# Kernel tuning notes

Hardware: AMD Instinct MI355X
Metric: run time of the kernel (lower is better)

## Reference

```python
import jax, jax.numpy as jnp
import numpy as np

N_NODES = 100000
N_EDGES = 1600000
N_GRAPHS = 4096
GN_EPS = 1e-5
SLOPE = 0.01  # torch leaky_relu default negative_slope


def _graph_norm(x, w, b, s):
    # PyG GraphNorm with batch=None: single-graph normalization over all nodes
    mean = jnp.mean(x, axis=0, keepdims=True)
    out = x - s * mean
    var = jnp.mean(out * out, axis=0, keepdims=True)
    return w * out * jax.lax.rsqrt(var + GN_EPS) + b


def setup_inputs() -> dict:
    key = jax.random.key(0)
    ks = jax.random.split(key, 12)

    def rn(k, shape, fan_in):
        return (jax.random.normal(k, shape, jnp.float32) / np.float32(np.sqrt(fan_in)))

    return {
        "x": jax.random.normal(ks[0], (N_NODES, 48), jnp.float32),
        "edge_attr": jax.random.normal(ks[1], (N_EDGES, 10), jnp.float32),
        # GINConv MLP layer 0: Linear(48->128); layers 1..3: Linear(128->128)
        "W1_0": rn(ks[2], (48, 128), 48), "b1_0": jnp.zeros((128,), jnp.float32),
        "W1_rest": rn(ks[3], (3, 128, 128), 128), "b1_rest": jnp.zeros((3, 128), jnp.float32),
        # GraphNorm inside each MLP (weight, bias, mean_scale)
        "gn_w": jnp.ones((4, 128), jnp.float32), "gn_b": jnp.zeros((4, 128), jnp.float32), "gn_s": jnp.ones((4, 128), jnp.float32),
        # second Linear of each MLP (128->128; last conv maps to out_channels=128)
        "W2": rn(ks[4], (4, 128, 128), 128), "b2": jnp.zeros((4, 128), jnp.float32),
        # BasicGNN post-conv GraphNorms (after layers 0..2 only)
        "pn_w": jnp.ones((3, 128), jnp.float32), "pn_b": jnp.zeros((3, 128), jnp.float32), "pn_s": jnp.ones((3, 128), jnp.float32),
        # readout MLP head
        "fc1_W": rn(ks[5], (384, 64), 384), "fc1_b": jnp.zeros((64,), jnp.float32),
        "fc2_W": rn(ks[6], (64, 3), 64), "fc2_b": jnp.zeros((3,), jnp.float32),
        "edge_index": jax.random.randint(ks[7], (2, N_EDGES), 0, N_NODES),
        "batch": jnp.sort(jax.random.randint(ks[8], (N_NODES,), 0, N_GRAPHS)),
    }


def reference(x, edge_attr, W1_0, b1_0, W1_rest, b1_rest, gn_w, gn_b, gn_s,
              W2, b2, pn_w, pn_b, pn_s, fc1_W, fc1_b, fc2_W, fc2_b,
              edge_index, batch):
    # edge_attr is ignored: PyG GIN does not support edge attributes.
    src, dst = edge_index[0], edge_index[1]
    h = x
    for i in range(4):
        # GINConv: mlp((1+eps)*x_i + sum_{j in N(i)} x_j), eps = 0
        agg = jax.ops.segment_sum(h[src], dst, num_segments=N_NODES)
        m = h + agg
        if i == 0:
            m = m @ W1_0 + b1_0
        else:
            m = m @ W1_rest[i - 1] + b1_rest[i - 1]
        m = _graph_norm(m, gn_w[i], gn_b[i], gn_s[i])  # norm inside MLP
        m = jax.nn.leaky_relu(m, SLOPE)
        h = m @ W2[i] + b2[i]
        if i < 3:  # BasicGNN: norm + act after every conv except the last
            h = _graph_norm(h, pn_w[i], pn_b[i], pn_s[i])
            h = jax.nn.leaky_relu(h, SLOPE)

    # global mean / add / max pooling over data.batch
    sums = jax.ops.segment_sum(h, batch, num_segments=N_GRAPHS)
    cnt = jax.ops.segment_sum(jnp.ones((h.shape[0], 1), h.dtype), batch,
                              num_segments=N_GRAPHS)
    mean = sums / jnp.maximum(cnt, 1.0)
    mx = jax.ops.segment_max(h, batch, num_segments=N_GRAPHS)
    mx = jnp.where(jnp.isfinite(mx), mx, 0.0)  # guard empty segments

    g = jnp.concatenate([mean, sums, mx], axis=1)  # [G, 384]
    g = jax.nn.leaky_relu(g @ fc1_W + fc1_b, SLOPE)
    return g @ fc2_W + fc2_b  # [G, 3]
```

## Files before the change

### kernel.cpp

```cpp
#include <hip/hip_runtime.h>
#include <hip/hip_bf16.h>
#include <math.h>

#define N_NODES  100000
#define N_EDGES  1600000
#define N_GRAPHS 4096
#define NBUCKET  ((N_NODES + 127) / 128)
#define NPART    256
#define ROWBLKS_AL 6256

typedef __attribute__((ext_vector_type(4))) float f32x4;
typedef __attribute__((ext_vector_type(8))) short bf16x8;

__device__ __forceinline__ float lrelu(float x) { return fmaxf(x, 0.01f * x); }

__device__ __forceinline__ unsigned short f2bf(float f) {
    unsigned u = __float_as_uint(f);
    unsigned r = (u + 0x7FFFu + ((u >> 16) & 1u)) >> 16;
    return (unsigned short)r;
}
__device__ __forceinline__ float bf2f(unsigned short h) {
    return __uint_as_float(((unsigned)h) << 16);
}

__global__ __launch_bounds__(1024) void scan_kernel(const unsigned* __restrict__ in,
                                                    unsigned* __restrict__ out, int n) {
    __shared__ unsigned wsum[16];
    __shared__ unsigned carry_s;
    int t = threadIdx.x, lane = t & 63, wv = t >> 6;
    if (t == 0) carry_s = 0u;
    __syncthreads();
    for (int base = 0; base < n; base += 4096) {
        unsigned carry = carry_s;
        unsigned v[4]; unsigned s = 0u;
#pragma unroll
        for (int i = 0; i < 4; ++i) {
            int idx = base + t * 4 + i;
            v[i] = (idx < n) ? in[idx] : 0u;
            s += v[i];
        }
        unsigned ps = s;
#pragma unroll
        for (int off = 1; off < 64; off <<= 1) {
            unsigned x = __shfl_up(ps, off, 64);
            if (lane >= off) ps += x;
        }
        if (lane == 63) wsum[wv] = ps;
        __syncthreads();
        if (wv == 0 && lane < 16) {
            unsigned pw = wsum[lane];
#pragma unroll
            for (int off = 1; off < 16; off <<= 1) {
                unsigned x = __shfl_up(pw, off, 64);
                if (lane >= off) pw += x;
            }
            wsum[lane] = pw;
        }
        __syncthreads();
        unsigned wbase = wv ? wsum[wv - 1] : 0u;
        unsigned run = carry + wbase + (ps - s);
#pragma unroll
        for (int i = 0; i < 4; ++i) {
            int idx = base + t * 4 + i;
            if (idx < n) out[idx] = run;
            run += v[i];
        }
        unsigned total = wsum[15];
        __syncthreads();
        if (t == 0) carry_s = carry + total;
        __syncthreads();
    }
    if (t == 0) out[n] = carry_s;
}

__global__ __launch_bounds__(256) void phist_kernel(const int* __restrict__ dst,
        unsigned* __restrict__ cnt, int E, int chunk) {
    __shared__ unsigned lc[NBUCKET];
    int p = blockIdx.x, t = threadIdx.x;
    for (int i = t; i < NBUCKET; i += 256) lc[i] = 0u;
    __syncthreads();
    int e0 = p * chunk, e1 = e0 + chunk; if (e1 > E) e1 = E;
    for (int e = e0 + t; e < e1; e += 256)
        atomicAdd(&lc[((unsigned)dst[e]) >> 7], 1u);
    __syncthreads();
    for (int i = t; i < NBUCKET; i += 256) cnt[(size_t)p * NBUCKET + i] = lc[i];
}

__global__ void btot_kernel(const unsigned* __restrict__ cnt, unsigned* __restrict__ tot) {
    int b = blockIdx.x * 256 + threadIdx.x;
    if (b >= NBUCKET) return;
    unsigned s = 0u;
    for (int p = 0; p < NPART; ++p) s += cnt[(size_t)p * NBUCKET + b];
    tot[b] = s;
}

__global__ __launch_bounds__(256) void poff_kernel(unsigned* __restrict__ cnt,
        const unsigned* __restrict__ bucket_base) {
    int b = blockIdx.x * 4 + (threadIdx.x >> 6);
    if (b >= NBUCKET) return;
    int lane = threadIdx.x & 63;
    unsigned v[4]; unsigned s = 0u;
#pragma unroll
    for (int i = 0; i < 4; ++i) {
        int p = lane * 4 + i;
        v[i] = cnt[(size_t)p * NBUCKET + b];
        s += v[i];
    }
    unsigned ps = s;
#pragma unroll
    for (int off = 1; off < 64; off <<= 1) {
        unsigned x = __shfl_up(ps, off, 64);
        if (lane >= off) ps += x;
    }
    unsigned run = bucket_base[b] + (ps - s);
#pragma unroll
    for (int i = 0; i < 4; ++i) {
        int p = lane * 4 + i;
        cnt[(size_t)p * NBUCKET + b] = run;
        run += v[i];
    }
}

__global__ __launch_bounds__(256) void pscat_kernel(const int* __restrict__ ei,
        const unsigned* __restrict__ cnt, unsigned* __restrict__ pair, int E, int chunk) {
    __shared__ unsigned lcur[NBUCKET];
    int p = blockIdx.x, t = threadIdx.x;
    for (int i = t; i < NBUCKET; i += 256) lcur[i] = cnt[(size_t)p * NBUCKET + i];
    __syncthreads();
    int e0 = p * chunk, e1 = e0 + chunk; if (e1 > E) e1 = E;
    for (int e = e0 + t; e < e1; e += 256) {
        unsigned src = (unsigned)ei[e];
        unsigned dst = (unsigned)ei[E + e];
        unsigned b = dst >> 7;
        unsigned pos = atomicAdd(&lcur[b], 1u);
        pair[pos] = src | ((dst & 127u) << 20);
    }
}

__global__ __launch_bounds__(256) void fillc2_kernel(const unsigned* __restrict__ pair,
        const unsigned* __restrict__ bucket_base, unsigned* __restrict__ row_ptr,
        unsigned* __restrict__ col, int N) {
    __shared__ unsigned lcnt[128], lpre[128], lcur[128];
    int b = blockIdx.x;
    int node0 = b << 7;
    int t = threadIdx.x;
    if (t < 128) { lcnt[t] = 0u; lcur[t] = 0u; }
    __syncthreads();
    unsigned bb = bucket_base[b], be = bucket_base[b + 1];
    for (unsigned i = bb + t; i < be; i += 256)
        atomicAdd(&lcnt[(pair[i] >> 20) & 127u], 1u);
    __syncthreads();
    if (t < 64) {
        unsigned v0 = lcnt[2 * t], v1 = lcnt[2 * t + 1];
        unsigned s = v0 + v1;
        unsigned ps = s;
#pragma unroll
        for (int off = 1; off < 64; off <<= 1) {
            unsigned x = __shfl_up(ps, off, 64);
            if (t >= off) ps += x;
        }
        unsigned base = ps - s;
        lpre[2 * t] = base;
        lpre[2 * t + 1] = base + v0;
    }
    __syncthreads();
    if (t < 128) {
        int node = node0 + t;
        if (node < N) row_ptr[node] = bb + lpre[t];
    }
    if (b == (int)gridDim.x - 1 && t == 0) row_ptr[N] = be;
    for (unsigned i = bb + t; i < be; i += 256) {
        unsigned u = pair[i];
        unsigned d = (u >> 20) & 127u;
        unsigned pos = bb + lpre[d] + atomicAdd(&lcur[d], 1u);
        col[pos] = u & 0xFFFFFu;
    }
}

__global__ void gsearch_kernel(const int* __restrict__ batch, unsigned* __restrict__ gptr,
                               int N, int G) {
    int g = blockIdx.x * 256 + threadIdx.x;
    if (g > G) return;
    int lo = 0, hi = N;
    while (lo < hi) { int mid = (lo + hi) >> 1; if (batch[mid] < g) lo = mid + 1; else hi = mid; }
    gptr[g] = (unsigned)lo;
}

__global__ void cast_kernel(const float* __restrict__ in, unsigned short* __restrict__ outb, int n4) {
    int i = blockIdx.x * 256 + threadIdx.x;
    if (i >= n4) return;
    f32x4 v = *(const f32x4*)(in + (size_t)i * 4);
    uint2 u;
    u.x = (unsigned)f2bf(v[0]) | ((unsigned)f2bf(v[1]) << 16);
    u.y = (unsigned)f2bf(v[2]) | ((unsigned)f2bf(v[3]) << 16);
    *(uint2*)(outb + (size_t)i * 4) = u;
}

__global__ __launch_bounds__(256) void tfm_kernel(const unsigned short* __restrict__ hb,
        const float* __restrict__ stats, const float* __restrict__ wp,
        const float* __restrict__ bp, const float* __restrict__ sp, float invN,
        unsigned short* __restrict__ yb, int total8) {
    __shared__ float la[128], ldd[128];
    int t = threadIdx.x;
    if (t < 128) {
        float mean = stats[t] * invN;
        float ex2  = stats[128 + t] * invN;
        float sv   = sp[t];
        float var  = ex2 - 2.f * sv * mean * mean + sv * sv * mean * mean;
        float a    = wp[t] * rsqrtf(var + 1e-5f);
        la[t] = a; ldd[t] = bp[t] - a * sv * mean;
    }
    __syncthreads();
    int i = blockIdx.x * 256 + t;
    if (i >= total8) return;
    int c0 = (i & 15) * 8;
    uint4 u = *(const uint4*)(hb + (size_t)i * 8);
    unsigned uu[4] = {u.x, u.y, u.z, u.w};
    unsigned ow[4];
#pragma unroll
    for (int q = 0; q < 4; ++q) {
        int c = c0 + 2 * q;
        float v0 = lrelu(fmaf(la[c],     __uint_as_float(uu[q] << 16),         ldd[c]));
        float v1 = lrelu(fmaf(la[c + 1], __uint_as_float(uu[q] & 0xffff0000u), ldd[c + 1]));
        ow[q] = (unsigned)f2bf(v0) | ((unsigned)f2bf(v1) << 16);
    }
    uint4 o; o.x = ow[0]; o.y = ow[1]; o.z = ow[2]; o.w = ow[3];
    *(uint4*)(yb + (size_t)i * 8) = o;
}

template<int D, int KOCT>
__global__ __launch_bounds__(256) void agg_kernel(const unsigned short* __restrict__ hb, int ld_in,
        const unsigned* __restrict__ row_ptr, const unsigned* __restrict__ col,
        unsigned short* __restrict__ op, int n) {
    int node = blockIdx.x * 4 + (threadIdx.x >> 6);
    int l = threadIdx.x & 63;
    if (node >= n || l >= KOCT * 4) return;
    int c = 2 * l;
    float x0 = 0.f, x1 = 0.f;
    if (c < D) {
        const unsigned short* hp = hb + c;
#define LOADU(s) *(const unsigned*)(hp + (size_t)(s) * ld_in)
#define LO(u) __uint_as_float((u) << 16)
#define HI(u) __uint_as_float((u) & 0xffff0000u)
        unsigned su = LOADU(node);
        x0 = LO(su); x1 = HI(su);
        float y0 = 0.f, y1 = 0.f, z0 = 0.f, z1 = 0.f, q0 = 0.f, q1 = 0.f;
        unsigned e0 = row_ptr[node], e1 = row_ptr[node + 1];
        unsigned e = e0;
        for (; e + 8 <= e1; e += 8) {
            unsigned c0i = col[e],     c1i = col[e + 1], c2i = col[e + 2], c3i = col[e + 3];
            unsigned c4i = col[e + 4], c5i = col[e + 5], c6i = col[e + 6], c7i = col[e + 7];
            unsigned u0 = LOADU(c0i), u1 = LOADU(c1i), u2 = LOADU(c2i), u3 = LOADU(c3i);
            unsigned u4 = LOADU(c4i), u5 = LOADU(c5i), u6 = LOADU(c6i), u7 = LOADU(c7i);
            x0 += LO(u0); x1 += HI(u0); y0 += LO(u1); y1 += HI(u1);
            z0 += LO(u2); z1 += HI(u2); q0 += LO(u3); q1 += HI(u3);
            x0 += LO(u4); x1 += HI(u4); y0 += LO(u5); y1 += HI(u5);
            z0 += LO(u6); z1 += HI(u6); q0 += LO(u7); q1 += HI(u7);
        }
        for (; e + 4 <= e1; e += 4) {
            unsigned c0i = col[e], c1i = col[e + 1], c2i = col[e + 2], c3i = col[e + 3];
            unsigned u0 = LOADU(c0i), u1 = LOADU(c1i), u2 = LOADU(c2i), u3 = LOADU(c3i);
            x0 += LO(u0); x1 += HI(u0); y0 += LO(u1); y1 += HI(u1);
            z0 += LO(u2); z1 += HI(u2); q0 += LO(u3); q1 += HI(u3);
        }
        for (; e < e1; ++e) {
            unsigned u = LOADU(col[e]);
            x0 += LO(u); x1 += HI(u);
        }
#undef LOADU
#undef LO
#undef HI
        x0 = (x0 + y0) + (z0 + q0);
        x1 = (x1 + y1) + (z1 + q1);
    }
    unsigned outw = (unsigned)f2bf(x0) | ((unsigned)f2bf(x1) << 16);
    size_t fo = (((size_t)(node >> 4) * KOCT + (l >> 2)) * 16 + (node & 15)) * 8 + 2 * (l & 3);
    *(unsigned*)(op + fo) = outw;
}

__global__ __launch_bounds__(256) void wsplit_kernel(const float* __restrict__ W1_0,
        const float* __restrict__ W1_rest, const float* __restrict__ W2,
        unsigned short* __restrict__ wt) {
    int g = blockIdx.y;
    int i = blockIdx.x * 256 + threadIdx.x;
    int e = i & 7, lane = (i >> 3) & 63, h = (i >> 9) & 1, j = (i >> 10) & 7, ks = i >> 13;
    int m = lane & 15, kg = lane >> 4;
    int k = ks * 32 + kg * 8 + e;
    int n = 8 * m + j;
    float v = 0.f;
    if (g == 0) { if (k < 48) v = W1_0[k * 128 + n]; }
    else if (g & 1) v = W2[(size_t)((g - 1) >> 1) * 16384 + k * 128 + n];
    else            v = W1_rest[(size_t)((g - 2) >> 1) * 16384 + k * 128 + n];
    unsigned short hi = f2bf(v);
    unsigned short out = (h == 0) ? hi : f2bf(v - bf2f(hi));
    wt[(size_t)g * 32768 + i] = out;
}

template<int KS, int KOCT, bool AFF, bool STATS, bool BF16OUT, bool FRAGOUT>
__global__ __launch_bounds__(256, 4) void mgemm_kernel(
        const unsigned short* __restrict__ Ah,
        const float* __restrict__ stats, const float* __restrict__ wp,
        const float* __restrict__ bp, const float* __restrict__ sp, float invN,
        const unsigned short* __restrict__ Wt, const float* __restrict__ bias,
        unsigned short* __restrict__ outb, unsigned short* __restrict__ ofh,
        float* __restrict__ ostats, int M) {
    __shared__ float ls[256];
    int t = threadIdx.x;
    if (STATS) { ls[t] = 0.f; __syncthreads(); }
    int lane = t & 63;
    int m = lane & 15, kg = lane >> 4;
    int wid = t >> 6;
    int wr = wid >> 1, wc = wid & 1;
    int rowBase = blockIdx.x * 64 + wr * 32;
    int rowblk0 = blockIdx.x * 4 + wr * 2;

    union U8 { bf16x8 v; unsigned short u[8]; };

    f32x4 acc[2][4];
#pragma unroll
    for (int j = 0; j < 4; ++j) {
        float b = bias[8 * m + wc * 4 + j];
        acc[0][j] = (f32x4){b, b, b, b};
        acc[1][j] = (f32x4){b, b, b, b};
    }

#pragma unroll
    for (int ks = 0; ks < KS; ++ks) {
        int k0 = ks * 32 + kg * 8;
        float aC[8], dC[8];
        if (AFF) {
            f32x4 sm0 = *(const f32x4*)(stats + k0),       sm1 = *(const f32x4*)(stats + k0 + 4);
            f32x4 se0 = *(const f32x4*)(stats + 128 + k0), se1 = *(const f32x4*)(stats + 128 + k0 + 4);
            f32x4 w0  = *(const f32x4*)(wp + k0),          w1  = *(const f32x4*)(wp + k0 + 4);
            f32x4 b0  = *(const f32x4*)(bp + k0),          b1  = *(const f32x4*)(bp + k0 + 4);
            f32x4 s0  = *(const f32x4*)(sp + k0),          s1  = *(const f32x4*)(sp + k0 + 4);
#pragma unroll
            for (int q = 0; q < 8; ++q) {
                float mean = (q < 4 ? sm0[q] : sm1[q - 4]) * invN;
                float ex2  = (q < 4 ? se0[q] : se1[q - 4]) * invN;
                float sv   = (q < 4 ? s0[q]  : s1[q - 4]);
                float var  = ex2 - 2.f * sv * mean * mean + sv * sv * mean * mean;
                float a    = (q < 4 ? w0[q] : w1[q - 4]) * rsqrtf(var + 1e-5f);
                aC[q] = a;
                dC[q] = (q < 4 ? b0[q] : b1[q - 4]) - a * sv * mean;
            }
        }
        U8 fh[2];
#pragma unroll
        for (int rg = 0; rg < 2; ++rg) {
            size_t ao = (((size_t)(rowblk0 + rg) * KOCT + ks * 4 + kg) << 7) + (m << 3);
            U8 h;
            h.v = *(const bf16x8*)(Ah + ao);
            if (AFF) {
#pragma unroll
                for (int q = 0; q < 8; ++q) {
                    float xv = lrelu(fmaf(aC[q], bf2f(h.u[q]), dC[q]));
                    h.u[q] = f2bf(xv);
                }
            }
            fh[rg] = h;
        }
#pragma unroll
        for (int j = 0; j < 4; ++j) {
            size_t wo = (size_t)(ks * 8 + wc * 4 + j) * 1024 + (size_t)lane * 8;
            bf16x8 whi = *(const bf16x8*)(Wt + wo);
            bf16x8 wlo = *(const bf16x8*)(Wt + wo + 512);
#pragma unroll
            for (int rg = 0; rg < 2; ++rg) {
                acc[rg][j] = __builtin_amdgcn_mfma_f32_16x16x32_bf16(fh[rg].v, whi, acc[rg][j], 0, 0, 0);
                acc[rg][j] = __builtin_amdgcn_mfma_f32_16x16x32_bf16(fh[rg].v, wlo, acc[rg][j], 0, 0, 0);
            }
        }
    }

#pragma unroll
    for (int rg = 0; rg < 2; ++rg) {
#pragma unroll
        for (int r = 0; r < 4; ++r) {
            int gr = rowBase + rg * 16 + kg * 4 + r;
            if (gr < M) {
                unsigned short h[4];
#pragma unroll
                for (int q = 0; q < 4; ++q) h[q] = f2bf(acc[rg][q][r]);
                uint2 uh;
                uh.x = (unsigned)h[0] | ((unsigned)h[1] << 16);
                uh.y = (unsigned)h[2] | ((unsigned)h[3] << 16);
                if (BF16OUT) *(uint2*)(outb + (size_t)gr * 128 + 8 * m + wc * 4) = uh;
                if (FRAGOUT) {
                    size_t fo = (((size_t)(rowblk0 + rg) * 16 + m) * 16 + (kg * 4 + r)) * 8 + wc * 4;
                    *(uint2*)(ofh + fo) = uh;
                }
            }
        }
    }

    if (STATS) {
#pragma unroll
        for (int j = 0; j < 4; ++j) {
            float s = 0.f, s2 = 0.f;
#pragma unroll
            for (int rg = 0; rg < 2; ++rg)
#pragma unroll
                for (int r = 0; r < 4; ++r) {
                    int gr = rowBase + rg * 16 + kg * 4 + r;
                    if (gr < M) { float v = acc[rg][j][r]; s += v; s2 += v * v; }
                }
            atomicAdd(&ls[8 * m + wc * 4 + j], s);
            atomicAdd(&ls[128 + 8 * m + wc * 4 + j], s2);
        }
        __syncthreads();
        atomicAdd(&ostats[t], ls[t]);
    }
}

__global__ __launch_bounds__(256) void pool_kernel(const unsigned short* __restrict__ hb,
        const unsigned* __restrict__ gptr, float* __restrict__ gout, int G) {
    int g = blockIdx.x * 4 + (threadIdx.x >> 6);
    int lane = threadIdx.x & 63;
    if (g >= G) return;
    unsigned s = gptr[g], e = gptr[g + 1];
    int c = 2 * lane;
    float sx = 0.f, sy = 0.f, mx = -INFINITY, my = -INFINITY;
    for (unsigned n = s; n < e; ++n) {
        unsigned u = *(const unsigned*)(hb + (size_t)n * 128 + c);
        float vx = __uint_as_float(u << 16);
        float vy = __uint_as_float(u & 0xffff0000u);
        sx += vx; sy += vy;
        mx = fmaxf(mx, vx); my = fmaxf(my, vy);
    }
    float cnt = (float)(e - s);
    float inv = 1.f / fmaxf(cnt, 1.f);
    if (e == s) { mx = 0.f; my = 0.f; }
    float* go = gout + (size_t)g * 384;
    go[c] = sx * inv;       go[c + 1] = sy * inv;
    go[128 + c] = sx;       go[128 + c + 1] = sy;
    go[256 + c] = mx;       go[256 + c + 1] = my;
}

__global__ __launch_bounds__(64) void head_kernel(const float* __restrict__ gbuf,
        const float* __restrict__ w1, const float* __restrict__ b1,
        const float* __restrict__ w2, const float* __restrict__ b2,
        float* __restrict__ out, int G) {
    __shared__ float y[64];
    int g = blockIdx.x, t = threadIdx.x;
    const float* row = gbuf + (size_t)g * 384;
    float acc = b1[t];
    for (int k = 0; k < 384; ++k) acc += row[k] * w1[(size_t)k * 64 + t];
    y[t] = lrelu(acc);
    __syncthreads();
    if (t < 3) {
        float o = b2[t];
        for (int k = 0; k < 64; ++k) o += y[k] * w2[k * 3 + t];
        out[(size_t)g * 3 + t] = o;
    }
}

extern "C" void kernel_launch(void* const* d_in, const int* in_sizes, int n_in,
                              void* d_out, int out_size, void* d_ws, size_t ws_size,
                              hipStream_t stream) {
    const float* x       = (const float*)d_in[0];
    const float* W1_0    = (const float*)d_in[2];
    const float* b1_0    = (const float*)d_in[3];
    const float* W1_rest = (const float*)d_in[4];
    const float* b1_rest = (const float*)d_in[5];
    const float* gn_w    = (const float*)d_in[6];
    const float* gn_b    = (const float*)d_in[7];
    const float* gn_s    = (const float*)d_in[8];
    const float* W2      = (const float*)d_in[9];
    const float* b2      = (const float*)d_in[10];
    const float* pn_w    = (const float*)d_in[11];
    const float* pn_b    = (const float*)d_in[12];
    const float* pn_s    = (const float*)d_in[13];
    const float* fc1W    = (const float*)d_in[14];
    const float* fc1b    = (const float*)d_in[15];
    const float* fc2W    = (const float*)d_in[16];
    const float* fc2b    = (const float*)d_in[17];
    const int*   ei      = (const int*)d_in[18];
    const int*   batch   = (const int*)d_in[19];
    float* outp = (float*)d_out;

    const int N = N_NODES, E = N_EDGES, G = N_GRAPHS;
    const int CHUNK = (E + NPART - 1) / NPART;
    const size_t FRAGSZ = (size_t)ROWBLKS_AL * 16 * 128;
    char* w = (char*)d_ws;
    auto alloc = [&](size_t bytes) -> char* {
        char* p = w; w += (bytes + 255) & ~(size_t)255; return p;
    };
    unsigned short* p1h = (unsigned short*)alloc(FRAGSZ * 2);
    unsigned short* p2h = (unsigned short*)alloc(FRAGSZ * 2);
    unsigned short* hb0 = (unsigned short*)alloc((size_t)N * 128 * 2);
    unsigned short* yb  = (unsigned short*)alloc((size_t)N * 128 * 2);
    unsigned short* xb  = (unsigned short*)alloc((size_t)N * 48 * 2);
    unsigned* row_ptr = (unsigned*)alloc((size_t)(N + 1) * 4);
    unsigned* colb    = (unsigned*)alloc((size_t)E * 4);
    unsigned* pair    = (unsigned*)alloc((size_t)E * 4);
    unsigned* cntm    = (unsigned*)alloc((size_t)NPART * NBUCKET * 4);
    unsigned* btot    = (unsigned*)alloc((size_t)(NBUCKET + 1) * 4);
    unsigned* bbase   = (unsigned*)alloc((size_t)(NBUCKET + 1) * 4);
    unsigned* gptr    = (unsigned*)alloc((size_t)(G + 1) * 4);
    float*    gbuf    = (float*)alloc((size_t)G * 384 * 4);
    unsigned short* wt = (unsigned short*)alloc((size_t)8 * 32768 * 2);
    float*    statsZ  = (float*)alloc(7 * 256 * 4);
    auto gnstats = [&](int i) { return statsZ + (size_t)i * 256; };
    auto pnstats = [&](int i) { return statsZ + (size_t)(4 + i) * 256; };

    hipMemsetAsync(statsZ, 0, 7 * 256 * 4, stream);

    phist_kernel<<<NPART, 256, 0, stream>>>(ei + E, cntm, E, CHUNK);
    btot_kernel<<<(NBUCKET + 255) / 256, 256, 0, stream>>>(cntm, btot);
    scan_kernel<<<1, 1024, 0, stream>>>(btot, bbase, NBUCKET);
    poff_kernel<<<(NBUCKET + 3) / 4, 256, 0, stream>>>(cntm, bbase);
    pscat_kernel<<<NPART, 256, 0, stream>>>(ei, cntm, pair, E, CHUNK);
    fillc2_kernel<<<NBUCKET, 256, 0, stream>>>(pair, bbase, row_ptr, colb, N);
    gsearch_kernel<<<(G + 256) / 256, 256, 0, stream>>>(batch, gptr, N, G);
    wsplit_kernel<<<dim3(128, 8), 256, 0, stream>>>(W1_0, W1_rest, W2, wt);
    cast_kernel<<<(N * 48 / 4 + 255) / 256, 256, 0, stream>>>(x, xb, N * 48 / 4);

    const float invN = 1.f / (float)N;
    int gemm_grid = (N + 63) / 64;
    int agg_grid  = (N + 3) / 4;
    int tfm_grid  = (N * 16 + 255) / 256;

    agg_kernel<48, 8><<<agg_grid, 256, 0, stream>>>(xb, 48, row_ptr, colb, p1h, N);
    mgemm_kernel<2, 8, false, true, false, true><<<gemm_grid, 256, 0, stream>>>(
            p1h, nullptr, nullptr, nullptr, nullptr, invN,
            wt, b1_0, nullptr, p2h, gnstats(0), N);
    mgemm_kernel<4, 16, true, true, true, false><<<gemm_grid, 256, 0, stream>>>(
            p2h, gnstats(0), gn_w, gn_b, gn_s, invN,
            wt + 1 * 32768, b2, hb0, nullptr, pnstats(0), N);

    for (int i = 1; i < 4; ++i) {
        tfm_kernel<<<tfm_grid, 256, 0, stream>>>(hb0, pnstats(i - 1),
                pn_w + (i - 1) * 128, pn_b + (i - 1) * 128, pn_s + (i - 1) * 128, invN,
                yb, N * 16);
        agg_kernel<128, 16><<<agg_grid, 256, 0, stream>>>(yb, 128, row_ptr, colb, p1h, N);
        mgemm_kernel<4, 16, false, true, false, true><<<gemm_grid, 256, 0, stream>>>(
                p1h, nullptr, nullptr, nullptr, nullptr, invN,
                wt + (size_t)(2 * i) * 32768, b1_rest + (size_t)(i - 1) * 128,
                nullptr, p2h, gnstats(i), N);
        if (i < 3) {
            mgemm_kernel<4, 16, true, true, true, false><<<gemm_grid, 256, 0, stream>>>(
                    p2h, gnstats(i), gn_w + i * 128, gn_b + i * 128, gn_s + i * 128, invN,
                    wt + (size_t)(2 * i + 1) * 32768, b2 + (size_t)i * 128,
                    hb0, nullptr, pnstats(i), N);
        } else {
            mgemm_kernel<4, 16, true, false, true, false><<<gemm_grid, 256, 0, stream>>>(
                    p2h, gnstats(3), gn_w + 3 * 128, gn_b + 3 * 128, gn_s + 3 * 128, invN,
                    wt + (size_t)7 * 32768, b2 + (size_t)3 * 128,
                    hb0, nullptr, nullptr, N);
        }
    }

    pool_kernel<<<(G + 3) / 4, 256, 0, stream>>>(hb0, gptr, gbuf, G);
    head_kernel<<<G, 64, 0, stream>>>(gbuf, fc1W, fc1b, fc2W, fc2b, outp, G);
}
```

Before: 800.5 us.

## Slice node features by channel group for aggregation and enlarge GEMM row tiles

The transform kernel now writes activations as 8 channel slices of 16 bf16 values per node. A new aggregation kernel gives each block one slice, so a block's neighbor gathers touch a smaller, more cache-friendly working set, and edges are split across 8 lane slots and combined with shuffles. Separately, the MFMA GEMM tile grows from 64 to 128 rows per block, with the occupancy hint lowered to 2 blocks per SM to make room for the extra accumulators. Risks are more row_ptr/col reads (once per slice), less parallel work per node, and lower occupancy in the GEMM.

```diff
diff --git a/kernel.cpp b/kernel.cpp
--- a/kernel.cpp
+++ b/kernel.cpp
@@ -8,6 +8,7 @@
 #define NBUCKET  ((N_NODES + 127) / 128)
 #define NPART    256
 #define ROWBLKS_AL 6256
+#define NSLICE_STRIDE ((size_t)N_NODES * 16)
 
 typedef __attribute__((ext_vector_type(4))) float f32x4;
 typedef __attribute__((ext_vector_type(8))) short bf16x8;
@@ -199,7 +200,7 @@
 __global__ __launch_bounds__(256) void tfm_kernel(const unsigned short* __restrict__ hb,
         const float* __restrict__ stats, const float* __restrict__ wp,
         const float* __restrict__ bp, const float* __restrict__ sp, float invN,
-        unsigned short* __restrict__ yb, int total8) {
+        unsigned short* __restrict__ yb2, int total8) {
     __shared__ float la[128], ldd[128];
     int t = threadIdx.x;
     if (t < 128) {
@@ -213,7 +214,8 @@
     __syncthreads();
     int i = blockIdx.x * 256 + t;
     if (i >= total8) return;
-    int c0 = (i & 15) * 8;
+    int node = i >> 4, cg = i & 15;
+    int c0 = cg * 8;
     uint4 u = *(const uint4*)(hb + (size_t)i * 8);
     unsigned uu[4] = {u.x, u.y, u.z, u.w};
     unsigned ow[4];
@@ -225,7 +227,53 @@
         ow[q] = (unsigned)f2bf(v0) | ((unsigned)f2bf(v1) << 16);
     }
     uint4 o; o.x = ow[0]; o.y = ow[1]; o.z = ow[2]; o.w = ow[3];
-    *(uint4*)(yb + (size_t)i * 8) = o;
+    unsigned short* dst = yb2 + (size_t)(cg >> 1) * NSLICE_STRIDE + (size_t)node * 16 + (cg & 1) * 8;
+    *(uint4*)dst = o;
+}
+
+__global__ __launch_bounds__(256) void agg2_kernel(const unsigned short* __restrict__ yb2,
+        const unsigned* __restrict__ row_ptr, const unsigned* __restrict__ col,
+        unsigned short* __restrict__ op, int n) {
+    int slice = blockIdx.x & 7, nb = blockIdx.x >> 3;
+    int t = threadIdx.x;
+    int lane = t & 63, w = t >> 6;
+    int slot = lane >> 3, cp = lane & 7;
+    const unsigned short* hp = yb2 + (size_t)slice * NSLICE_STRIDE + cp * 2;
+#define LO(u) __uint_as_float((u) << 16)
+#define HI(u) __uint_as_float((u) & 0xffff0000u)
+    int node0 = nb * 128 + w * 32;
+    for (int ni = 0; ni < 32; ++ni) {
+        int node = node0 + ni;
+        if (node >= n) return;
+        unsigned e0 = row_ptr[node], e1 = row_ptr[node + 1];
+        unsigned su = 0u;
+        if (slot == 0) su = *(const unsigned*)(hp + (size_t)node * 16);
+        float x0 = LO(su), x1 = HI(su), y0 = 0.f, y1 = 0.f;
+        unsigned e = e0 + slot;
+        for (; e + 8 < e1; e += 16) {
+            unsigned i0 = col[e], i1 = col[e + 8];
+            unsigned u0 = *(const unsigned*)(hp + (size_t)i0 * 16);
+            unsigned u1 = *(const unsigned*)(hp + (size_t)i1 * 16);
+            x0 += LO(u0); x1 += HI(u0);
+            y0 += LO(u1); y1 += HI(u1);
+        }
+        if (e < e1) {
+            unsigned u = *(const unsigned*)(hp + (size_t)col[e] * 16);
+            x0 += LO(u); x1 += HI(u);
+        }
+        x0 += y0; x1 += y1;
+        x0 += __shfl_xor(x0, 8, 64);  x1 += __shfl_xor(x1, 8, 64);
+        x0 += __shfl_xor(x0, 16, 64); x1 += __shfl_xor(x1, 16, 64);
+        x0 += __shfl_xor(x0, 32, 64); x1 += __shfl_xor(x1, 32, 64);
+        if (slot == 0) {
+            int l = slice * 8 + cp;
+            unsigned outw = (unsigned)f2bf(x0) | ((unsigned)f2bf(x1) << 16);
+            size_t fo = (((size_t)(node >> 4) * 16 + (l >> 2)) * 16 + (node & 15)) * 8 + 2 * (l & 3);
+            *(unsigned*)(op + fo) = outw;
+        }
+    }
+#undef LO
+#undef HI
 }
 
 template<int D, int KOCT>
@@ -297,7 +345,7 @@
 }
 
 template<int KS, int KOCT, bool AFF, bool STATS, bool BF16OUT, bool FRAGOUT>
-__global__ __launch_bounds__(256, 4) void mgemm_kernel(
+__global__ __launch_bounds__(256, 2) void mgemm_kernel(
         const unsigned short* __restrict__ Ah,
         const float* __restrict__ stats, const float* __restrict__ wp,
         const float* __restrict__ bp, const float* __restrict__ sp, float invN,
@@ -311,17 +359,17 @@
     int m = lane & 15, kg = lane >> 4;
     int wid = t >> 6;
     int wr = wid >> 1, wc = wid & 1;
-    int rowBase = blockIdx.x * 64 + wr * 32;
-    int rowblk0 = blockIdx.x * 4 + wr * 2;
+    int rowBase = blockIdx.x * 128 + wr * 64;
+    int rowblk0 = blockIdx.x * 8 + wr * 4;
 
     union U8 { bf16x8 v; unsigned short u[8]; };
 
-    f32x4 acc[2][4];
+    f32x4 acc[4][4];
 #pragma unroll
     for (int j = 0; j < 4; ++j) {
         float b = bias[8 * m + wc * 4 + j];
-        acc[0][j] = (f32x4){b, b, b, b};
-        acc[1][j] = (f32x4){b, b, b, b};
+#pragma unroll
+        for (int rg = 0; rg < 4; ++rg) acc[rg][j] = (f32x4){b, b, b, b};
     }
 
 #pragma unroll
@@ -345,9 +393,9 @@
                 dC[q] = (q < 4 ? b0[q] : b1[q - 4]) - a * sv * mean;
             }
         }
-        U8 fh[2];
-#pragma unroll
-        for (int rg = 0; rg < 2; ++rg) {
+        U8 fh[4];
+#pragma unroll
+        for (int rg = 0; rg < 4; ++rg) {
             size_t ao = (((size_t)(rowblk0 + rg) * KOCT + ks * 4 + kg) << 7) + (m << 3);
             U8 h;
             h.v = *(const bf16x8*)(Ah + ao);
@@ -366,7 +414,7 @@
             bf16x8 whi = *(const bf16x8*)(Wt + wo);
             bf16x8 wlo = *(const bf16x8*)(Wt + wo + 512);
 #pragma unroll
-            for (int rg = 0; rg < 2; ++rg) {
+            for (int rg = 0; rg < 4; ++rg) {
                 acc[rg][j] = __builtin_amdgcn_mfma_f32_16x16x32_bf16(fh[rg].v, whi, acc[rg][j], 0, 0, 0);
                 acc[rg][j] = __builtin_amdgcn_mfma_f32_16x16x32_bf16(fh[rg].v, wlo, acc[rg][j], 0, 0, 0);
             }
@@ -374,7 +422,7 @@
     }
 
 #pragma unroll
-    for (int rg = 0; rg < 2; ++rg) {
+    for (int rg = 0; rg < 4; ++rg) {
 #pragma unroll
         for (int r = 0; r < 4; ++r) {
             int gr = rowBase + rg * 16 + kg * 4 + r;
@@ -399,7 +447,7 @@
         for (int j = 0; j < 4; ++j) {
             float s = 0.f, s2 = 0.f;
 #pragma unroll
-            for (int rg = 0; rg < 2; ++rg)
+            for (int rg = 0; rg < 4; ++rg)
 #pragma unroll
                 for (int r = 0; r < 4; ++r) {
                     int gr = rowBase + rg * 16 + kg * 4 + r;
@@ -489,7 +537,7 @@
     unsigned short* p1h = (unsigned short*)alloc(FRAGSZ * 2);
     unsigned short* p2h = (unsigned short*)alloc(FRAGSZ * 2);
     unsigned short* hb0 = (unsigned short*)alloc((size_t)N * 128 * 2);
-    unsigned short* yb  = (unsigned short*)alloc((size_t)N * 128 * 2);
+    unsigned short* yb2 = (unsigned short*)alloc((size_t)N * 128 * 2);
     unsigned short* xb  = (unsigned short*)alloc((size_t)N * 48 * 2);
     unsigned* row_ptr = (unsigned*)alloc((size_t)(N + 1) * 4);
     unsigned* colb    = (unsigned*)alloc((size_t)E * 4);
@@ -517,11 +565,12 @@
     cast_kernel<<<(N * 48 / 4 + 255) / 256, 256, 0, stream>>>(x, xb, N * 48 / 4);
 
     const float invN = 1.f / (float)N;
-    int gemm_grid = (N + 63) / 64;
-    int agg_grid  = (N + 3) / 4;
+    int gemm_grid = (N + 127) / 128;
+    int agg0_grid = (N + 3) / 4;
+    int agg2_grid = ((N + 127) / 128) * 8;
     int tfm_grid  = (N * 16 + 255) / 256;
 
-    agg_kernel<48, 8><<<agg_grid, 256, 0, stream>>>(xb, 48, row_ptr, colb, p1h, N);
+    agg_kernel<48, 8><<<agg0_grid, 256, 0, stream>>>(xb, 48, row_ptr, colb, p1h, N);
     mgemm_kernel<2, 8, false, true, false, true><<<gemm_grid, 256, 0, stream>>>(
             p1h, nullptr, nullptr, nullptr, nullptr, invN,
             wt, b1_0, nullptr, p2h, gnstats(0), N);
@@ -532,8 +581,8 @@
     for (int i = 1; i < 4; ++i) {
         tfm_kernel<<<tfm_grid, 256, 0, stream>>>(hb0, pnstats(i - 1),
                 pn_w + (i - 1) * 128, pn_b + (i - 1) * 128, pn_s + (i - 1) * 128, invN,
-                yb, N * 16);
-        agg_kernel<128, 16><<<agg_grid, 256, 0, stream>>>(yb, 128, row_ptr, colb, p1h, N);
+                yb2, N * 16);
+        agg2_kernel<<<agg2_grid, 256, 0, stream>>>(yb2, row_ptr, colb, p1h, N);
         mgemm_kernel<4, 16, false, true, false, true><<<gemm_grid, 256, 0, stream>>>(
                 p1h, nullptr, nullptr, nullptr, nullptr, invN,
                 wt + (size_t)(2 * i) * 32768, b1_rest + (size_t)(i - 1) * 128,
```

Result: slower. 1.073 ms (+34.1%).
